# Performance work log

Measured on AMD Instinct MI355X. Metric: run time of the kernel, lower is better.

## Reference

```python
import jax, jax.numpy as jnp
import numpy as np

NUM_HEADS = 16
WINDOW_SIZE = (7, 7, 7)  # (D, H, W)


def _relative_position_index(window_size):
    # Faithful numpy replication of SwinWindowAttention.get_relative_position_index (3D branch).
    D, H, W = window_size
    w, d, h = np.meshgrid(np.arange(W), np.arange(D), np.arange(H), indexing='ij')
    coords = np.stack([d, h, w], axis=0)              # [3, W, D, H]
    flat = coords.reshape(3, -1)                       # [3, N]
    rel = flat[:, :, None] - flat[:, None, :]          # [3, N, N]
    rel = rel.transpose(1, 2, 0)                       # [N, N, 3]
    offsets = []
    mult = 1
    for size in reversed(window_size):
        offsets.insert(0, mult)
        mult *= 2 * size - 1
    offsets = np.asarray(offsets, dtype=np.int32)
    rel = rel + np.asarray([s - 1 for s in window_size])
    return np.sum(rel.astype(np.int32) * offsets, axis=-1).astype(np.int32)  # [N, N]


def setup_inputs() -> dict:
    key = jax.random.key(0)
    ks = jax.random.split(key, 6)
    B, N, C = 64, 343, 512          # B = true_batch * num_windows
    NW = 8                           # mask_size; B % NW == 0
    TBL = 13 * 13 * 13              # prod(2*s - 1) = 2197
    x = jax.random.normal(ks[0], (B, N, C), dtype=jnp.float32)
    mask = jnp.zeros((NW, N, N), dtype=jnp.float32)  # shift mask (0 / -inf pattern in practice)
    w_qkv = jax.random.normal(ks[1], (C, 3 * C), dtype=jnp.float32) * (C ** -0.5)
    b_qkv = jnp.zeros((3 * C,), dtype=jnp.float32)
    w_proj = jax.random.normal(ks[2], (C, C), dtype=jnp.float32) * (C ** -0.5)
    b_proj = jnp.zeros((C,), dtype=jnp.float32)
    bias_table = jax.random.normal(ks[3], (TBL, NUM_HEADS), dtype=jnp.float32) * 0.02
    rel_index = jnp.asarray(_relative_position_index(WINDOW_SIZE))  # [N, N] int32
    return {"x": x, "mask": mask, "w_qkv": w_qkv, "b_qkv": b_qkv,
            "w_proj": w_proj, "b_proj": b_proj, "bias_table": bias_table,
            "rel_index": rel_index}


def reference(x, mask, w_qkv, b_qkv, w_proj, b_proj, bias_table, rel_index):
    B, N, C = x.shape
    H = NUM_HEADS
    hd = C // H
    scale = hd ** -0.5
    qkv = x @ w_qkv + b_qkv                              # [B, N, 3C]
    qkv = qkv.reshape(B, N, 3, H, hd).transpose(2, 0, 3, 1, 4)  # [3, B, H, N, hd]
    q, k, v = qkv[0] * scale, qkv[1], qkv[2]
    attn = jnp.einsum('bhnd,bhmd->bhnm', q, k)           # [B, H, N, N]
    # relative position bias: gather [N,N,H] -> [H,N,N]
    bias = bias_table[rel_index].transpose(2, 0, 1)
    attn = attn + bias[None]
    nw = mask.shape[0]
    attn = attn.reshape(B // nw, nw, H, N, N) + mask[:, None, :, :]
    attn = attn.reshape(B, H, N, N)
    attn = jax.nn.softmax(attn, axis=-1)
    out = jnp.einsum('bhnm,bhmd->bhnd', attn, v)         # [B, H, N, hd]
    out = out.transpose(0, 2, 1, 3).reshape(B, N, C)
    return out @ w_proj + b_proj
```

## Files before the change

### kernel.cpp

```cpp
#include <hip/hip_runtime.h>

typedef __bf16 bf16_t;
typedef __bf16 bf16x4 __attribute__((ext_vector_type(4)));
typedef __bf16 bf16x8 __attribute__((ext_vector_type(8)));
typedef short  s16x4  __attribute__((ext_vector_type(4)));
typedef float  f32x4  __attribute__((ext_vector_type(4)));

#define NUM_B 64
#define SEQ   343
#define CH    512
#define NH    16
#define HDIM  32
#define NWIN  8
#define C3    1536
#define MTOT  (NUM_B * SEQ)
#define MPAD  22016
#define NTILES 22
#define NPAD  352
#define NN    (SEQ * SEQ)
#define MB_TILES 172
#define QSCALE 0.17677669529663687f
#define LOG2E  1.4426950408889634f

__device__ __forceinline__ f32x4 mfma16(bf16x8 a, bf16x8 b, f32x4 c) {
    return __builtin_amdgcn_mfma_f32_16x16x32_bf16(a, b, c, 0, 0, 0);
}

__device__ __forceinline__ f32x4 mfma16k16(bf16x4 a, bf16x4 b, f32x4 c) {
    return __builtin_amdgcn_mfma_f32_16x16x16bf16_1k(
        __builtin_bit_cast(s16x4, a), __builtin_bit_cast(s16x4, b), c, 0, 0, 0);
}

__device__ __forceinline__ bf16x8 bf8_zero() {
    bf16x8 v;
#pragma unroll
    for (int i = 0; i < 8; ++i) v[i] = (bf16_t)0.f;
    return v;
}

__device__ __forceinline__ bf16x8 pack8(const float4& a, const float4& b) {
    bf16x8 v;
    v[0] = (bf16_t)a.x; v[1] = (bf16_t)a.y; v[2] = (bf16_t)a.z; v[3] = (bf16_t)a.w;
    v[4] = (bf16_t)b.x; v[5] = (bf16_t)b.y; v[6] = (bf16_t)b.z; v[7] = (bf16_t)b.w;
    return v;
}

__device__ __forceinline__ float f4get(const float4& v, int i) {
    return i == 0 ? v.x : i == 1 ? v.y : i == 2 ? v.z : v.w;
}

__device__ __forceinline__ void gload16(const void* g, void* l) {
    __builtin_amdgcn_global_load_lds(
        (const __attribute__((address_space(1))) void*)g,
        (__attribute__((address_space(3))) void*)l, 16, 0, 0);
}

__global__ __launch_bounds__(256) void swin_prep(
        const float* __restrict__ X, const float* __restrict__ Wq,
        const float* __restrict__ Wp, const float* __restrict__ bias_table,
        const int* __restrict__ rel_index, const float* __restrict__ mask,
        bf16_t* __restrict__ Xb, bf16_t* __restrict__ WTq, bf16_t* __restrict__ WTp,
        bf16_t* __restrict__ comb) {
    __shared__ __align__(16) float shbuf[32 * 33];
    const int bid = blockIdx.x, t = threadIdx.x;
    if (bid < 5504) {
        size_t e = ((size_t)bid * 256 + t) * 8;
        bf16x8 v;
        if (e < (size_t)MTOT * CH) {
            const float4* p = reinterpret_cast<const float4*>(&X[e]);
            v = pack8(p[0], p[1]);
        } else v = bf8_zero();
        *reinterpret_cast<bf16x8*>(&Xb[e]) = v;
        return;
    }
    if (bid < 6528) {
        float (*tile)[33] = reinterpret_cast<float(*)[33]>(shbuf);
        const float* src; bf16_t* dst; int srcN, k0, n0;
        if (bid < 5504 + 768) {
            int b2 = bid - 5504;
            k0 = (b2 % 16) * 32; n0 = (b2 / 16) * 32;
            src = Wq; dst = WTq; srcN = C3;
        } else {
            int b2 = bid - 5504 - 768;
            k0 = (b2 % 16) * 32; n0 = (b2 / 16) * 32;
            src = Wp; dst = WTp; srcN = CH;
        }
        int r = t >> 3, c4 = (t & 7) * 4;
        const float4 u = *reinterpret_cast<const float4*>(&src[(size_t)(k0 + r) * srcN + n0 + c4]);
        tile[r][c4 + 0] = u.x; tile[r][c4 + 1] = u.y; tile[r][c4 + 2] = u.z; tile[r][c4 + 3] = u.w;
        __syncthreads();
        bf16x4 o;
#pragma unroll
        for (int j = 0; j < 4; ++j) o[j] = (bf16_t)tile[c4 + j][r];
        *reinterpret_cast<bf16x4*>(&dst[(size_t)(n0 + r) * CH + k0 + c4]) = o;
        return;
    }
    const int cid = bid - 6528;
    const int ntq = cid % 6, mt = (cid / 6) % NTILES, w = cid / (6 * NTILES);
    const int nt = ntq * 4 + (t >> 6);
    if (nt >= NTILES) return;
    const int lane = t & 63;
    const int lm = lane & 15, g = lane >> 4;
    const int gm = mt * 16 + lm;
    const bool gmok = gm < SEQ;

    bool ok[4]; int idx[4]; float mv[4];
#pragma unroll
    for (int r = 0; r < 4; ++r) {
        int gn = nt * 16 + 4 * g + r;
        ok[r] = gmok && (gn < SEQ);
        int a = ok[r] ? gm * SEQ + gn : 0;
        idx[r] = rel_index[a];
        mv[r] = ok[r] ? mask[(size_t)w * NN + a] : 0.f;
    }
    const size_t outb = ((size_t)mt * NTILES + nt) * 64 + lane;
    bf16x4* combv = reinterpret_cast<bf16x4*>(comb);
#pragma unroll
    for (int hq = 0; hq < 4; ++hq) {
        float4 b0 = *reinterpret_cast<const float4*>(&bias_table[idx[0] * NH + hq * 4]);
        float4 b1 = *reinterpret_cast<const float4*>(&bias_table[idx[1] * NH + hq * 4]);
        float4 b2 = *reinterpret_cast<const float4*>(&bias_table[idx[2] * NH + hq * 4]);
        float4 b3 = *reinterpret_cast<const float4*>(&bias_table[idx[3] * NH + hq * 4]);
#pragma unroll
        for (int hh = 0; hh < 4; ++hh) {
            int h = hq * 4 + hh;
            bf16x4 o;
            o[0] = ok[0] ? (bf16_t)((f4get(b0, hh) + mv[0]) * LOG2E) : (bf16_t)(-1e30f);
            o[1] = ok[1] ? (bf16_t)((f4get(b1, hh) + mv[1]) * LOG2E) : (bf16_t)(-1e30f);
            o[2] = ok[2] ? (bf16_t)((f4get(b2, hh) + mv[2]) * LOG2E) : (bf16_t)(-1e30f);
            o[3] = ok[3] ? (bf16_t)((f4get(b3, hh) + mv[3]) * LOG2E) : (bf16_t)(-1e30f);
            combv[(size_t)(h * 8 + w) * (NTILES * NTILES * 64) + outb] = o;
        }
    }
}

template <int NB, bool QKV>
__global__ __launch_bounds__(256) void swin_gemm(
        const bf16_t* __restrict__ A, const bf16_t* __restrict__ BT,
        const float* __restrict__ bias, void* __restrict__ outv) {
    __shared__ __align__(16) bf16_t sh[3][2][128 * 32];
    const int nwg8 = MB_TILES * NB / 8;
    int bid = blockIdx.x;
    bid = (bid & 7) * nwg8 + (bid >> 3);
    const int nb = bid % NB, mb = bid / NB;
    const int m0 = mb * 128, n0 = nb * 128;
    const int t = threadIdx.x, wid = t >> 6, lane = t & 63;
    const int wr = wid >> 1, wc = wid & 1;
    const int lm = lane & 15, g = lane >> 4;
    const int swr = ((lane >> 2) ^ (lane >> 4)) & 3;
    const bf16_t* gA = &A[(size_t)(m0 + wid * 32 + (lane >> 2)) * CH + (((lane & 3) ^ swr) << 3)];
    const bf16_t* gB = &BT[(size_t)(n0 + wid * 32 + (lane >> 2)) * CH + (((lane & 3) ^ swr) << 3)];
    const int soff = ((g ^ ((lm ^ (lm >> 2)) & 3)) << 3);

    f32x4 acc[4][4];
#pragma unroll
    for (int i = 0; i < 4; ++i)
#pragma unroll
        for (int j = 0; j < 4; ++j) {
            acc[i][j][0] = 0.f; acc[i][j][1] = 0.f; acc[i][j][2] = 0.f; acc[i][j][3] = 0.f;
        }

#define STAGE(tile, buf)                                                          \
    do {                                                                          \
        const int _k0 = (tile) * 32;                                              \
        gload16(gA + _k0,               &sh[(buf)][0][(wid * 32 + 0) * 32]);      \
        gload16(gA + _k0 + 16 * CH,     &sh[(buf)][0][(wid * 32 + 16) * 32]);     \
        gload16(gB + _k0,               &sh[(buf)][1][(wid * 32 + 0) * 32]);      \
        gload16(gB + _k0 + 16 * CH,     &sh[(buf)][1][(wid * 32 + 16) * 32]);     \
    } while (0)

    STAGE(0, 0);
    STAGE(1, 1);
#pragma unroll
    for (int kt = 0; kt < 16; ++kt) {
        if (kt <= 14) asm volatile("s_waitcnt vmcnt(4)" ::: "memory");
        else          asm volatile("s_waitcnt vmcnt(0)" ::: "memory");
        __builtin_amdgcn_s_barrier();
        __builtin_amdgcn_sched_barrier(0);
        if (kt <= 13) STAGE(kt + 2, (kt + 2) % 3);
        const int buf = kt % 3;
        bf16x8 a[4], b[4];
#pragma unroll
        for (int i = 0; i < 4; ++i)
            a[i] = *reinterpret_cast<const bf16x8*>(&sh[buf][0][(wr * 64 + i * 16 + lm) * 32 + soff]);
#pragma unroll
        for (int j = 0; j < 4; ++j)
            b[j] = *reinterpret_cast<const bf16x8*>(&sh[buf][1][(wc * 64 + j * 16 + lm) * 32 + soff]);
        __builtin_amdgcn_s_setprio(1);
#pragma unroll
        for (int i = 0; i < 4; ++i)
#pragma unroll
            for (int j = 0; j < 4; ++j)
                acc[i][j] = mfma16(a[i], b[j], acc[i][j]);
        __builtin_amdgcn_s_setprio(0);
    }
#undef STAGE
    __syncthreads();

    const int rb = (lane >> 4) << 2;
    if (QKV) {
        bf16_t* Cs = &sh[0][0][0];
#pragma unroll
        for (int j = 0; j < 4; ++j) {
            int col = wc * 64 + j * 16 + lm;
            float bv = bias[n0 + col];
            float sc = (n0 + col < CH) ? (QSCALE * LOG2E) : 1.0f;
#pragma unroll
            for (int i = 0; i < 4; ++i)
#pragma unroll
                for (int r = 0; r < 4; ++r)
                    Cs[(wr * 64 + i * 16 + rb + r) * 136 + col] = (bf16_t)((acc[i][j][r] + bv) * sc);
        }
        __syncthreads();
        bf16_t* outp = (bf16_t*)outv;
#pragma unroll
        for (int it = 0; it < 8; ++it) {
            int row = (t >> 4) + it * 16;
            int c8 = (t & 15) * 8;
            bf16x8 v = *reinterpret_cast<const bf16x8*>(&Cs[row * 136 + c8]);
            int grow = m0 + row;
            if (grow < MTOT)
                *reinterpret_cast<bf16x8*>(&outp[(size_t)grow * (NB * 128) + n0 + c8]) = v;
        }
    } else {
        float* fCs = reinterpret_cast<float*>(&sh[0][0][0]);
        float* outp = (float*)outv;
#pragma unroll
        for (int half = 0; half < 2; ++half) {
            __syncthreads();
            if (wr == half) {
#pragma unroll
                for (int j = 0; j < 4; ++j) {
                    int col = wc * 64 + j * 16 + lm;
                    float bv = bias[n0 + col];
#pragma unroll
                    for (int i = 0; i < 4; ++i)
#pragma unroll
                        for (int r = 0; r < 4; ++r)
                            fCs[(i * 16 + rb + r) * 128 + col] = acc[i][j][r] + bv;
                }
            }
            __syncthreads();
#pragma unroll
            for (int it = 0; it < 8; ++it) {
                int row = (t >> 5) + it * 8;
                int c4 = (t & 31) * 4;
                float4 v = *reinterpret_cast<const float4*>(&fCs[row * 128 + c4]);
                int grow = m0 + half * 64 + row;
                if (grow < MTOT)
                    *reinterpret_cast<float4*>(&outp[(size_t)grow * (NB * 128) + n0 + c4]) = v;
            }
        }
    }
}

__global__ __launch_bounds__(512, 6) void swin_attn(
        const bf16_t* __restrict__ qkv, const bf16_t* __restrict__ comb,
        bf16_t* __restrict__ attout) {
    __shared__ __align__(16) bf16_t Ksh[NPAD * 32];
    __shared__ __align__(16) bf16_t Vsh[32 * NPAD];
    const int t = threadIdx.x;
    const int bid = blockIdx.x;
    const int h = (bid & 127) >> 3;
    const int w = bid & 7;
    const int b = w + ((bid >> 7) << 3);
    const int plane = h * 8 + w;
    const int wid = t >> 6, lane = t & 63;
    const int lm = lane & 15, g = lane >> 4;
    const int lkb = g << 3;
    const size_t rowbase = (size_t)b * SEQ;

    for (int base = 0; base < SEQ; base += 128) {
        int n = base + (t >> 2);
        int db = (t & 3) << 3;
        if (n < SEQ) {
            bf16x8 kv = *reinterpret_cast<const bf16x8*>(&qkv[(rowbase + n) * C3 + CH + h * HDIM + db]);
            *reinterpret_cast<bf16x8*>(&Ksh[(n * 32 + db) ^ (((n >> 1) & 3) << 3)]) = kv;
            bf16x8 vv = *reinterpret_cast<const bf16x8*>(&qkv[(rowbase + n) * C3 + 2 * CH + h * HDIM + db]);
#pragma unroll
            for (int e = 0; e < 8; ++e) {
                int d = db + e;
                Vsh[(d * NPAD + n) ^ (((d >> 1) & 3) << 3)] = vv[e];
            }
        }
    }
    if (t < 36) {
        int n = SEQ + (t >> 2), db = (t & 3) << 3;
        *reinterpret_cast<bf16x8*>(&Ksh[(n * 32 + db) ^ (((n >> 1) & 3) << 3)]) = bf8_zero();
    }
    for (int i = t; i < 32 * 9; i += 512) {
        int d = i / 9, n = SEQ + (i % 9);
        Vsh[(d * NPAD + n) ^ (((d >> 1) & 3) << 3)] = (bf16_t)0.f;
    }
    __syncthreads();

    const int kswz = ((lm >> 1) & 3) << 3;
    const int kbase = (lm * 32 + lkb) ^ kswz;
    const int vb0e = (lm * NPAD + 4 * g) ^ kswz;
    const int vb0o = (lm * NPAD + 4 * g + 16) ^ kswz;
    const int vb1e = ((16 + lm) * NPAD + 4 * g) ^ kswz;
    const int vb1o = ((16 + lm) * NPAD + 4 * g + 16) ^ kswz;

    bf16x4 ones;
    ones[0] = (bf16_t)1.f; ones[1] = (bf16_t)1.f; ones[2] = (bf16_t)1.f; ones[3] = (bf16_t)1.f;

    for (int mt = wid; mt < NTILES; mt += 8) {
        const int m0 = mt * 16;
        bf16x8 qf = *reinterpret_cast<const bf16x8*>(&qkv[(rowbase + m0 + lm) * C3 + h * HDIM + lkb]);

        f32x4 o0 = {0.f, 0.f, 0.f, 0.f}, o1 = {0.f, 0.f, 0.f, 0.f};
        f32x4 osum = {0.f, 0.f, 0.f, 0.f};
        const bf16x4* cp = reinterpret_cast<const bf16x4*>(comb) + ((size_t)plane * NTILES + mt) * NTILES * 64;
#pragma unroll 2
        for (int nt = 0; nt < NTILES; ++nt) {
            bf16x4 cb = cp[nt * 64 + lane];
            bf16x8 kf = *reinterpret_cast<const bf16x8*>(&Ksh[kbase + nt * 512]);
            f32x4 z;
            z[0] = (float)cb[0]; z[1] = (float)cb[1]; z[2] = (float)cb[2]; z[3] = (float)cb[3];
            f32x4 s = mfma16(kf, qf, z);
            bf16x4 pa;
#pragma unroll
            for (int r = 0; r < 4; ++r)
                pa[r] = (bf16_t)__builtin_amdgcn_exp2f(s[r]);
            const int off = (nt >> 1) * 32;
            bf16x4 v0 = *reinterpret_cast<const bf16x4*>(&Vsh[((nt & 1) ? vb0o : vb0e) + off]);
            bf16x4 v1 = *reinterpret_cast<const bf16x4*>(&Vsh[((nt & 1) ? vb1o : vb1e) + off]);
            o0 = mfma16k16(pa, v0, o0);
            o1 = mfma16k16(pa, v1, o1);
            osum = mfma16k16(pa, ones, osum);
        }
#pragma unroll
        for (int r = 0; r < 4; ++r) {
            int gm = m0 + 4 * g + r;
            if (gm < SEQ) {
                float iv = 1.f / osum[r];
                attout[(rowbase + gm) * CH + h * HDIM + lm]      = (bf16_t)(o0[r] * iv);
                attout[(rowbase + gm) * CH + h * HDIM + 16 + lm] = (bf16_t)(o1[r] * iv);
            }
        }
    }
}

extern "C" void kernel_launch(void* const* d_in, const int* in_sizes, int n_in,
                              void* d_out, int out_size, void* d_ws, size_t ws_size,
                              hipStream_t stream) {
    const float* x          = (const float*)d_in[0];
    const float* mask       = (const float*)d_in[1];
    const float* w_qkv      = (const float*)d_in[2];
    const float* b_qkv      = (const float*)d_in[3];
    const float* w_proj     = (const float*)d_in[4];
    const float* b_proj     = (const float*)d_in[5];
    const float* bias_table = (const float*)d_in[6];
    const int*   rel_index  = (const int*)d_in[7];
    float* out = (float*)d_out;

    char* ws = (char*)d_ws;
    const size_t qkv_bytes = (size_t)MPAD * C3 * sizeof(bf16_t);
    const size_t xb_bytes  = (size_t)MPAD * CH * sizeof(bf16_t);
    const size_t wtq_bytes = (size_t)C3 * CH * sizeof(bf16_t);
    const size_t wtp_bytes = (size_t)CH * CH * sizeof(bf16_t);
    bf16_t* qkv    = (bf16_t*)ws;
    bf16_t* Xb     = (bf16_t*)(ws + qkv_bytes);
    bf16_t* attout = Xb;
    bf16_t* WTq    = (bf16_t*)(ws + qkv_bytes + xb_bytes);
    bf16_t* WTp    = (bf16_t*)(ws + qkv_bytes + xb_bytes + wtq_bytes);
    bf16_t* comb   = (bf16_t*)(ws + qkv_bytes + xb_bytes + wtq_bytes + wtp_bytes);

    const int prep_grid = 5504 + 768 + 256 + NWIN * NTILES * 6;
    hipLaunchKernelGGL(swin_prep, dim3(prep_grid), dim3(256), 0, stream,
                       x, w_qkv, w_proj, bias_table, rel_index, mask, Xb, WTq, WTp, comb);
    hipLaunchKernelGGL((swin_gemm<12, true>), dim3(MB_TILES * 12), dim3(256), 0, stream,
                       Xb, WTq, b_qkv, (void*)qkv);
    hipLaunchKernelGGL(swin_attn, dim3(NUM_B * NH), dim3(512), 0, stream,
                       qkv, comb, attout);
    hipLaunchKernelGGL((swin_gemm<4, false>), dim3(MB_TILES * 4), dim3(256), 0, stream,
                       attout, WTp, b_proj, (void*)out);
}
```

Measured before the change: 145.9 us.

## Pre-swizzle weights into MFMA fragment order and load B directly to registers

The prep kernel now writes the transposed bf16 weights in a fragment-major layout that matches the per-lane MFMA B operand order. The GEMM drops the LDS staging for B and instead loads B fragments straight from global memory into registers, prefetching the next k-step one iteration ahead. This halves LDS traffic and LDS footprint per block, which may raise occupancy. In exchange, each wave issues its own global loads for B with less cross-wave reuse, and register pressure rises from the double-buffered B fragments.

```diff
diff --git a/kernel.cpp b/kernel.cpp
--- a/kernel.cpp
+++ b/kernel.cpp
@@ -59,7 +59,7 @@
         const float* __restrict__ X, const float* __restrict__ Wq,
         const float* __restrict__ Wp, const float* __restrict__ bias_table,
         const int* __restrict__ rel_index, const float* __restrict__ mask,
-        bf16_t* __restrict__ Xb, bf16_t* __restrict__ WTq, bf16_t* __restrict__ WTp,
+        bf16_t* __restrict__ Xb, bf16_t* __restrict__ Bfq, bf16_t* __restrict__ Bfp,
         bf16_t* __restrict__ comb) {
     __shared__ __align__(16) float shbuf[32 * 33];
     const int bid = blockIdx.x, t = threadIdx.x;
@@ -76,23 +76,27 @@
     if (bid < 6528) {
         float (*tile)[33] = reinterpret_cast<float(*)[33]>(shbuf);
         const float* src; bf16_t* dst; int srcN, k0, n0;
-        if (bid < 5504 + 768) {
+        if (bid < 6272) {
             int b2 = bid - 5504;
             k0 = (b2 % 16) * 32; n0 = (b2 / 16) * 32;
-            src = Wq; dst = WTq; srcN = C3;
+            src = Wq; dst = Bfq; srcN = C3;
         } else {
-            int b2 = bid - 5504 - 768;
+            int b2 = bid - 6272;
             k0 = (b2 % 16) * 32; n0 = (b2 / 16) * 32;
-            src = Wp; dst = WTp; srcN = CH;
+            src = Wp; dst = Bfp; srcN = CH;
         }
         int r = t >> 3, c4 = (t & 7) * 4;
         const float4 u = *reinterpret_cast<const float4*>(&src[(size_t)(k0 + r) * srcN + n0 + c4]);
         tile[r][c4 + 0] = u.x; tile[r][c4 + 1] = u.y; tile[r][c4 + 2] = u.z; tile[r][c4 + 3] = u.w;
         __syncthreads();
+        const int sub = t >> 7, lane2 = (t >> 1) & 63, half = t & 1;
+        const int lm = lane2 & 15, g = lane2 >> 4;
         bf16x4 o;
 #pragma unroll
-        for (int j = 0; j < 4; ++j) o[j] = (bf16_t)tile[c4 + j][r];
-        *reinterpret_cast<bf16x4*>(&dst[(size_t)(n0 + r) * CH + k0 + c4]) = o;
+        for (int e = 0; e < 4; ++e)
+            o[e] = (bf16_t)tile[g * 8 + half * 4 + e][sub * 16 + lm];
+        const size_t off = ((size_t)(((n0 >> 4) + sub) * 16 + (k0 >> 5)) * 64 + lane2) * 8 + half * 4;
+        *reinterpret_cast<bf16x4*>(&dst[off]) = o;
         return;
     }
     const int cid = bid - 6528;
@@ -136,9 +140,9 @@
 
 template <int NB, bool QKV>
 __global__ __launch_bounds__(256) void swin_gemm(
-        const bf16_t* __restrict__ A, const bf16_t* __restrict__ BT,
+        const bf16_t* __restrict__ A, const bf16_t* __restrict__ Bf,
         const float* __restrict__ bias, void* __restrict__ outv) {
-    __shared__ __align__(16) bf16_t sh[3][2][128 * 32];
+    __shared__ __align__(16) bf16_t shraw[17408];
     const int nwg8 = MB_TILES * NB / 8;
     int bid = blockIdx.x;
     bid = (bid & 7) * nwg8 + (bid >> 3);
@@ -149,8 +153,8 @@
     const int lm = lane & 15, g = lane >> 4;
     const int swr = ((lane >> 2) ^ (lane >> 4)) & 3;
     const bf16_t* gA = &A[(size_t)(m0 + wid * 32 + (lane >> 2)) * CH + (((lane & 3) ^ swr) << 3)];
-    const bf16_t* gB = &BT[(size_t)(n0 + wid * 32 + (lane >> 2)) * CH + (((lane & 3) ^ swr) << 3)];
     const int soff = ((g ^ ((lm ^ (lm >> 2)) & 3)) << 3);
+    const bf16_t* gBf = &Bf[((size_t)((n0 >> 4) + wc * 4) * 16) * 512 + lane * 8];
 
     f32x4 acc[4][4];
 #pragma unroll
@@ -163,43 +167,52 @@
 #define STAGE(tile, buf)                                                          \
     do {                                                                          \
         const int _k0 = (tile) * 32;                                              \
-        gload16(gA + _k0,               &sh[(buf)][0][(wid * 32 + 0) * 32]);      \
-        gload16(gA + _k0 + 16 * CH,     &sh[(buf)][0][(wid * 32 + 16) * 32]);     \
-        gload16(gB + _k0,               &sh[(buf)][1][(wid * 32 + 0) * 32]);      \
-        gload16(gB + _k0 + 16 * CH,     &sh[(buf)][1][(wid * 32 + 16) * 32]);     \
+        gload16(gA + _k0,           &shraw[(buf) * 4096 + (wid * 32 + 0) * 32]);  \
+        gload16(gA + _k0 + 16 * CH, &shraw[(buf) * 4096 + (wid * 32 + 16) * 32]); \
     } while (0)
 
     STAGE(0, 0);
     STAGE(1, 1);
+    bf16x8 bc[4], bn[4];
+#pragma unroll
+    for (int j = 0; j < 4; ++j)
+        bc[j] = *reinterpret_cast<const bf16x8*>(gBf + (size_t)j * 8192);
+
 #pragma unroll
     for (int kt = 0; kt < 16; ++kt) {
-        if (kt <= 14) asm volatile("s_waitcnt vmcnt(4)" ::: "memory");
-        else          asm volatile("s_waitcnt vmcnt(0)" ::: "memory");
+        if (kt <= 14) asm volatile("s_waitcnt vmcnt(6)" ::: "memory");
+        else          asm volatile("s_waitcnt vmcnt(4)" ::: "memory");
         __builtin_amdgcn_s_barrier();
         __builtin_amdgcn_sched_barrier(0);
         if (kt <= 13) STAGE(kt + 2, (kt + 2) % 3);
+        if (kt <= 14) {
+#pragma unroll
+            for (int j = 0; j < 4; ++j)
+                bn[j] = *reinterpret_cast<const bf16x8*>(gBf + (size_t)j * 8192 + (kt + 1) * 512);
+        }
         const int buf = kt % 3;
-        bf16x8 a[4], b[4];
+        bf16x8 a[4];
 #pragma unroll
         for (int i = 0; i < 4; ++i)
-            a[i] = *reinterpret_cast<const bf16x8*>(&sh[buf][0][(wr * 64 + i * 16 + lm) * 32 + soff]);
-#pragma unroll
-        for (int j = 0; j < 4; ++j)
-            b[j] = *reinterpret_cast<const bf16x8*>(&sh[buf][1][(wc * 64 + j * 16 + lm) * 32 + soff]);
+            a[i] = *reinterpret_cast<const bf16x8*>(&shraw[buf * 4096 + (wr * 64 + i * 16 + lm) * 32 + soff]);
         __builtin_amdgcn_s_setprio(1);
 #pragma unroll
         for (int i = 0; i < 4; ++i)
 #pragma unroll
             for (int j = 0; j < 4; ++j)
-                acc[i][j] = mfma16(a[i], b[j], acc[i][j]);
+                acc[i][j] = mfma16(a[i], bc[j], acc[i][j]);
         __builtin_amdgcn_s_setprio(0);
+        if (kt <= 14) {
+#pragma unroll
+            for (int j = 0; j < 4; ++j) bc[j] = bn[j];
+        }
     }
 #undef STAGE
     __syncthreads();
 
     const int rb = (lane >> 4) << 2;
     if (QKV) {
-        bf16_t* Cs = &sh[0][0][0];
+        bf16_t* Cs = &shraw[0];
 #pragma unroll
         for (int j = 0; j < 4; ++j) {
             int col = wc * 64 + j * 16 + lm;
@@ -223,7 +236,7 @@
                 *reinterpret_cast<bf16x8*>(&outp[(size_t)grow * (NB * 128) + n0 + c8]) = v;
         }
     } else {
-        float* fCs = reinterpret_cast<float*>(&sh[0][0][0]);
+        float* fCs = reinterpret_cast<float*>(&shraw[0]);
         float* outp = (float*)outv;
 #pragma unroll
         for (int half = 0; half < 2; ++half) {
@@ -357,22 +370,22 @@
     char* ws = (char*)d_ws;
     const size_t qkv_bytes = (size_t)MPAD * C3 * sizeof(bf16_t);
     const size_t xb_bytes  = (size_t)MPAD * CH * sizeof(bf16_t);
-    const size_t wtq_bytes = (size_t)C3 * CH * sizeof(bf16_t);
-    const size_t wtp_bytes = (size_t)CH * CH * sizeof(bf16_t);
+    const size_t bfq_bytes = (size_t)C3 * CH * sizeof(bf16_t);
+    const size_t bfp_bytes = (size_t)CH * CH * sizeof(bf16_t);
     bf16_t* qkv    = (bf16_t*)ws;
     bf16_t* Xb     = (bf16_t*)(ws + qkv_bytes);
     bf16_t* attout = Xb;
-    bf16_t* WTq    = (bf16_t*)(ws + qkv_bytes + xb_bytes);
-    bf16_t* WTp    = (bf16_t*)(ws + qkv_bytes + xb_bytes + wtq_bytes);
-    bf16_t* comb   = (bf16_t*)(ws + qkv_bytes + xb_bytes + wtq_bytes + wtp_bytes);
+    bf16_t* Bfq    = (bf16_t*)(ws + qkv_bytes + xb_bytes);
+    bf16_t* Bfp    = (bf16_t*)(ws + qkv_bytes + xb_bytes + bfq_bytes);
+    bf16_t* comb   = (bf16_t*)(ws + qkv_bytes + xb_bytes + bfq_bytes + bfp_bytes);
 
     const int prep_grid = 5504 + 768 + 256 + NWIN * NTILES * 6;
     hipLaunchKernelGGL(swin_prep, dim3(prep_grid), dim3(256), 0, stream,
-                       x, w_qkv, w_proj, bias_table, rel_index, mask, Xb, WTq, WTp, comb);
+                       x, w_qkv, w_proj, bias_table, rel_index, mask, Xb, Bfq, Bfp, comb);
     hipLaunchKernelGGL((swin_gemm<12, true>), dim3(MB_TILES * 12), dim3(256), 0, stream,
-                       Xb, WTq, b_qkv, (void*)qkv);
+                       Xb, Bfq, b_qkv, (void*)qkv);
     hipLaunchKernelGGL(swin_attn, dim3(NUM_B * NH), dim3(512), 0, stream,
                        qkv, comb, attout);
     hipLaunchKernelGGL((swin_gemm<4, false>), dim3(MB_TILES * 4), dim3(256), 0, stream,
-                       attout, WTp, b_proj, (void*)out);
-}
+                       attout, Bfp, b_proj, (void*)out);
+}
```

Result: no change. 145.5 us (-0.3%).
